# Performance work log

Measured on AMD Instinct MI355X. Metric: run time of the kernel, lower is better.

Reference implementation:

```python
import jax, jax.numpy as jnp
import numpy as np

N_NODES = 100000
N_EDGES = 3200000
H, D = 3, 12  # heads, per-head dim; H*D == node_hidden_dim == 36
NEG_SLOPE = 0.2


def setup_inputs() -> dict:
    key = jax.random.key(0)
    ks = jax.random.split(key, 11)
    s = 0.1
    return {
        "node_features": jax.random.normal(ks[0], (N_NODES, 36), jnp.float32),
        "src": jax.random.randint(ks[1], (N_EDGES,), 0, N_NODES),
        "dst": jax.random.randint(ks[2], (N_EDGES,), 0, N_NODES),
        "lin0_w": jax.random.normal(ks[3], (36, 36), jnp.float32) * s,
        "lin0_b": jax.random.normal(ks[4], (36,), jnp.float32) * s,
        "fc_w": jax.random.normal(ks[5], (3, 36, 36), jnp.float32) * s,
        "attn_l": jax.random.normal(ks[6], (3, H, D), jnp.float32) * s,
        "attn_r": jax.random.normal(ks[7], (3, H, D), jnp.float32) * s,
        "gat_bias": jax.random.normal(ks[8], (3, 36), jnp.float32) * s,
        "out_w": jax.random.normal(ks[9], (36, 36), jnp.float32) * s,
        "out_b": jax.random.normal(ks[10], (36,), jnp.float32) * s,
    }


def _gat_layer(h, src, dst, fc_w, a_l, a_r, bias):
    n = h.shape[0]
    feat = (h @ fc_w).reshape(n, H, D)                      # (N,H,D)
    el = jnp.sum(feat * a_l, axis=-1)                       # (N,H)
    er = jnp.sum(feat * a_r, axis=-1)                       # (N,H)
    e = el[src] + er[dst]                                   # (E,H)
    e = jnp.where(e >= 0, e, NEG_SLOPE * e)                 # leaky_relu(0.2)
    # edge softmax over incoming edges of each dst node (numerically stable)
    m = jax.ops.segment_max(e, dst, num_segments=n)         # (N,H)
    m = jnp.where(jnp.isfinite(m), m, 0.0)                  # zero-degree guard
    ee = jnp.exp(e - m[dst])                                # (E,H)
    denom = jax.ops.segment_sum(ee, dst, num_segments=n)    # (N,H)
    alpha = ee / jnp.maximum(denom[dst], 1e-9)              # (E,H)
    msg = feat[src] * alpha[:, :, None]                     # (E,H,D)
    rst = jax.ops.segment_sum(msg, dst, num_segments=n)     # (N,H,D)
    # residual (Identity since in_feats == H*D) + bias, then ELU
    rst = rst + h.reshape(n, H, D) + bias.reshape(1, H, D)
    return jax.nn.elu(rst).reshape(n, H * D)


def reference(node_features, src, dst, lin0_w, lin0_b, fc_w, attn_l, attn_r, gat_bias, out_w, out_b):
    h = node_features @ lin0_w + lin0_b
    for l in range(3):
        h = _gat_layer(h, src, dst, fc_w[l], attn_l[l], attn_r[l], gat_bias[l])
    return h @ out_w + out_b
```

## Files before the change

### kernel.cpp

```cpp
#include <hip/hip_runtime.h>
#include <math.h>

#define HID 36
#define NH 3
#define HD 12
#define BSHIFT 13
#define NBUCK 13
#define PSHIFT 8
#define PCHUNK 8192
#define CSRCAP 4096

typedef _Float16 f16;


__global__ void hist2_kernel(const int* __restrict__ dst, int* __restrict__ M,
                             int E, int C, int np) {
    __shared__ int h[512];
    int t = threadIdx.x;
    int c = blockIdx.x;
    for (int i = t; i < 512; i += blockDim.x) h[i] = 0;
    __syncthreads();
    int i0 = c * PCHUNK;
    int i1 = min(i0 + PCHUNK, E);
    for (int i = i0 + t; i < i1; i += blockDim.x)
        atomicAdd(&h[dst[i] >> PSHIFT], 1);
    __syncthreads();
    for (int b = t; b < np; b += blockDim.x)
        M[(size_t)b * C + c] = h[b];
}

__global__ void base_scan_kernel(const int* __restrict__ M, int* __restrict__ BaseT,
                                 int* __restrict__ T, int C, int np) {
    __shared__ int tmp[512];
    int b = blockIdx.x;
    int t = threadIdx.x;
    int v = (t < C) ? M[(size_t)b * C + t] : 0;
    tmp[t] = v;
    __syncthreads();
    for (int ofs = 1; ofs < 512; ofs <<= 1) {
        int x = 0;
        if (t >= ofs) x = tmp[t - ofs];
        __syncthreads();
        tmp[t] += x;
        __syncthreads();
    }
    if (t < C) BaseT[(size_t)t * 512 + b] = tmp[t] - v;
    if (t == 511) T[b] = tmp[511];
}

__global__ void scan_small_kernel(const int* __restrict__ T, int* __restrict__ poff, int np) {
    __shared__ int tmp[512];
    int t = threadIdx.x;
    int v = (t < np) ? T[t] : 0;
    tmp[t] = v;
    __syncthreads();
    for (int ofs = 1; ofs < 512; ofs <<= 1) {
        int x = 0;
        if (t >= ofs) x = tmp[t - ofs];
        __syncthreads();
        tmp[t] += x;
        __syncthreads();
    }
    int excl = tmp[t] - v;
    if (t < np) poff[t] = excl;
    if (t == np - 1) poff[np] = excl + v;
}

__global__ void part_scatter_kernel(const int* __restrict__ src, const int* __restrict__ dst,
                                    const int* __restrict__ BaseT, const int* __restrict__ poff,
                                    int* __restrict__ part, int E, int np) {
    __shared__ int h[512];
    __shared__ int base[512];
    int t = threadIdx.x;
    int c = blockIdx.x;
    for (int i = t; i < 512; i += blockDim.x) h[i] = 0;
    for (int b = t; b < np; b += blockDim.x)
        base[b] = poff[b] + BaseT[(size_t)c * 512 + b];
    __syncthreads();
    int i0 = c * PCHUNK;
    int i1 = min(i0 + PCHUNK, E);
    for (int i = i0 + t; i < i1; i += blockDim.x) {
        int d = dst[i];
        int bin = d >> PSHIFT;
        int r = atomicAdd(&h[bin], 1);
        part[base[bin] + r] = (src[i] << PSHIFT) | (d & ((1 << PSHIFT) - 1));
    }
}

__global__ void bucket_csr_kernel(const int* __restrict__ part, const int* __restrict__ T,
                                  const int* __restrict__ poff,
                                  int* __restrict__ csr, int* __restrict__ off,
                                  int n, int E) {
    __shared__ int cnt[256 * NBUCK];
    __shared__ int psum[256];
    int p = blockIdx.x;
    int t = threadIdx.x;
    int dbase = p << PSHIFT;
    int nd = min(256, n - dbase);
    int nc = nd * NBUCK;
    for (int i = t; i < nc; i += blockDim.x) cnt[i] = 0;
    __syncthreads();
    int cnt_p = T[p];
    int e0 = poff[p];
    const int* pp = part + e0;
    for (int i = t; i < cnt_p; i += blockDim.x) {
        int e = pp[i];
        atomicAdd(&cnt[(e & 255) * NBUCK + ((e >> PSHIFT) >> BSHIFT)], 1);
    }
    __syncthreads();
    int sum = 0;
    if (t < nd) {
        for (int k = 0; k < NBUCK; ++k) {
            int c = cnt[t * NBUCK + k];
            cnt[t * NBUCK + k] = sum;
            sum += c;
        }
    }
    psum[t] = (t < nd) ? sum : 0;
    __syncthreads();
    for (int ofs = 1; ofs < 256; ofs <<= 1) {
        int x = 0;
        if (t >= ofs) x = psum[t - ofs];
        __syncthreads();
        psum[t] += x;
        __syncthreads();
    }
    int dexcl = (t > 0) ? psum[t - 1] : 0;
    int start = e0 + dexcl;
    if (t < nd) {
        for (int k = 0; k < NBUCK; ++k) cnt[t * NBUCK + k] += start;
        off[dbase + t] = start;
    }
    __syncthreads();
    for (int i = t; i < cnt_p; i += blockDim.x) {
        int e = pp[i];
        int s = e >> PSHIFT;
        int idx = (e & 255) * NBUCK + (s >> BSHIFT);
        int pos = atomicAdd(&cnt[idx], 1);
        csr[pos] = s * 48;
    }
    if (p == 0 && t == 0) off[n] = E;
}


__device__ __forceinline__ void edge_accum(uint4 qa, uint4 qb, float ern,
                                           float& denom, float* acc) {
    union { uint4 q[2]; f16 hx[16]; } v;
    v.q[0] = qa;
    v.q[1] = qb;
    float e = (float)v.hx[12] + ern;
    e = (e >= 0.f) ? e : 0.2f * e;
    float w = __expf(e);
    denom += w;
#pragma unroll
    for (int k = 0; k < HD; ++k) acc[k] += w * (float)v.hx[k];
}

template <bool FITS>
__device__ __forceinline__ void sweep_edges(const int* __restrict__ smbuf,
                                            const int* __restrict__ csre,
                                            int j, int jend, const f16* __restrict__ pb,
                                            float ern, float& denom, float* acc) {
    int m = jend - j;
    for (; m >= 4; m -= 4, j += 4) {
        int o0 = FITS ? smbuf[j]     : csre[j];
        int o1 = FITS ? smbuf[j + 1] : csre[j + 1];
        int o2 = FITS ? smbuf[j + 2] : csre[j + 2];
        int o3 = FITS ? smbuf[j + 3] : csre[j + 3];
        const uint4* r0 = (const uint4*)(pb + o0);
        const uint4* r1 = (const uint4*)(pb + o1);
        const uint4* r2 = (const uint4*)(pb + o2);
        const uint4* r3 = (const uint4*)(pb + o3);
        uint4 a0 = r0[0], b0 = r0[1];
        uint4 a1 = r1[0], b1 = r1[1];
        uint4 a2 = r2[0], b2 = r2[1];
        uint4 a3 = r3[0], b3 = r3[1];
        edge_accum(a0, b0, ern, denom, acc);
        edge_accum(a1, b1, ern, denom, acc);
        edge_accum(a2, b2, ern, denom, acc);
        edge_accum(a3, b3, ern, denom, acc);
    }
    for (; m > 0; --m, ++j) {
        int o = FITS ? smbuf[j] : csre[j];
        const uint4* r = (const uint4*)(pb + o);
        edge_accum(r[0], r[1], ern, denom, acc);
    }
}

__global__ void lin0tr_kernel(const float* __restrict__ x, const float* __restrict__ w0,
                              const float* __restrict__ b0, const float* __restrict__ fcw,
                              const float* __restrict__ al, const float* __restrict__ ar,
                              float* __restrict__ h, f16* __restrict__ packed,
                              float* __restrict__ er, int n) {
    __shared__ float W0[HID * HID];
    __shared__ float W1[HID * HID];
    __shared__ float Bs[HID], ALs[HID], ARs[HID];
    int t = threadIdx.x;
    for (int i = t; i < HID * HID; i += 256) { W0[i] = w0[i]; W1[i] = fcw[i]; }
    if (t < HID) { Bs[t] = b0[t]; ALs[t] = al[t]; ARs[t] = ar[t]; }
    __syncthreads();
    int node = blockIdx.x * 256 + t;
    if (node >= n) return;
    const float4* xp = (const float4*)(x + (size_t)node * HID);
    float h0[HID];
#pragma unroll
    for (int j = 0; j < HID; ++j) h0[j] = Bs[j];
#pragma unroll
    for (int kk = 0; kk < HID / 4; ++kk) {
        float4 xv = xp[kk];
        const float* w = &W0[(4 * kk) * HID];
#pragma unroll
        for (int j = 0; j < HID; ++j)
            h0[j] += xv.x * w[j] + xv.y * w[HID + j] + xv.z * w[2 * HID + j] + xv.w * w[3 * HID + j];
    }
    float* hp = h + (size_t)node * HID;
#pragma unroll
    for (int j = 0; j < HID; ++j) hp[j] = h0[j];
    float feat[HID];
#pragma unroll
    for (int j = 0; j < HID; ++j) feat[j] = 0.f;
#pragma unroll
    for (int k = 0; k < HID; ++k) {
        float hv = h0[k];
        const float* w = &W1[k * HID];
#pragma unroll
        for (int j = 0; j < HID; ++j) feat[j] += hv * w[j];
    }
    union { f16 hx[48]; uint4 q[6]; } u;
#pragma unroll
    for (int hh = 0; hh < NH; ++hh) {
        float sl = 0.f, sr = 0.f;
#pragma unroll
        for (int d = 0; d < HD; ++d) {
            sl += feat[hh * HD + d] * ALs[hh * HD + d];
            sr += feat[hh * HD + d] * ARs[hh * HD + d];
        }
#pragma unroll
        for (int d = 0; d < HD; ++d) u.hx[hh * 16 + d] = (f16)feat[hh * HD + d];
        u.hx[hh * 16 + 12] = (f16)sl;
        u.hx[hh * 16 + 13] = (f16)0.f;
        u.hx[hh * 16 + 14] = (f16)0.f;
        u.hx[hh * 16 + 15] = (f16)0.f;
        er[node * NH + hh] = sr;
    }
    uint4* prow = (uint4*)(packed + (size_t)node * 48);
#pragma unroll
    for (int q = 0; q < 6; ++q) prow[q] = u.q[q];
}

__global__ void __launch_bounds__(192)
aggtr_kernel(const f16* __restrict__ packed_in, const float* __restrict__ er_in,
             const float* __restrict__ hcur,
             const int* __restrict__ off, const int* __restrict__ csr,
             const float* __restrict__ bias, const float* __restrict__ wnext,
             const float* __restrict__ aln, const float* __restrict__ arn,
             float* __restrict__ hnext, f16* __restrict__ packed_out,
             float* __restrict__ er_out, int n) {
    __shared__ float Wsh[HID * HID];
    __shared__ float ALs[HID], ARs[HID];
    __shared__ int smbuf[CSRCAP];
    int t = threadIdx.x;
    for (int i = t; i < HID * HID; i += 192) Wsh[i] = wnext[i];
    if (t < HID) { ALs[t] = aln[t]; ARs[t] = arn[t]; }
    int ln = t / 3, hh = t - ln * 3;
    int nb0 = blockIdx.x * 64;
    int node = nb0 + ln;
    bool active = (node < n);

    int e0 = off[nb0];
    int e1 = off[min(nb0 + 64, n)];
    int span = e1 - e0;
    bool fits = (span <= CSRCAP);
    if (fits)
        for (int i = t; i < span; i += 192) smbuf[i] = csr[e0 + i];

    int j0 = 0, j1 = 0;
    float ern = 0.f;
    if (active) {
        j0 = off[node] - e0;
        j1 = off[node + 1] - e0;
        ern = er_in[node * NH + hh];
    }
    const f16* pb = packed_in + hh * 16;
    __syncthreads();

    float denom = 0.f;
    float acc[HD];
#pragma unroll
    for (int k = 0; k < HD; ++k) acc[k] = 0.f;

    if (fits) sweep_edges<true>(smbuf, csr + e0, j0, j1, pb, ern, denom, acc);
    else      sweep_edges<false>(smbuf, csr + e0, j0, j1, pb, ern, denom, acc);
    __syncthreads();

    float* hsh = (float*)smbuf;
    float v[HD];
#pragma unroll
    for (int k = 0; k < HD; ++k) v[k] = 0.f;
    if (active) {
        float inv = 1.f / fmaxf(denom, 1e-9f);
        int base = node * HID + hh * HD;
        const float4* hc = (const float4*)(hcur + base);
        float4 h0 = hc[0], h1 = hc[1], h2 = hc[2];
        float hres[HD] = {h0.x, h0.y, h0.z, h0.w, h1.x, h1.y, h1.z, h1.w, h2.x, h2.y, h2.z, h2.w};
#pragma unroll
        for (int k = 0; k < HD; ++k) {
            float x = acc[k] * inv + hres[k] + bias[hh * HD + k];
            v[k] = (x > 0.f) ? x : expm1f(x);
        }
        float4* hp = (float4*)(hnext + base);
        hp[0] = make_float4(v[0], v[1], v[2], v[3]);
        hp[1] = make_float4(v[4], v[5], v[6], v[7]);
        hp[2] = make_float4(v[8], v[9], v[10], v[11]);
    }
#pragma unroll
    for (int k = 0; k < HD; ++k) hsh[ln * 37 + hh * HD + k] = v[k];
    __syncthreads();

    float feat[HD];
#pragma unroll
    for (int d = 0; d < HD; ++d) feat[d] = 0.f;
    const float* hrow = &hsh[ln * 37];
#pragma unroll 4
    for (int k = 0; k < HID; ++k) {
        float hv = hrow[k];
        const float* w = &Wsh[k * HID + hh * HD];
#pragma unroll
        for (int d = 0; d < HD; ++d) feat[d] += hv * w[d];
    }
    if (!active) return;
    float sl = 0.f, sr = 0.f;
#pragma unroll
    for (int d = 0; d < HD; ++d) {
        sl += feat[d] * ALs[hh * HD + d];
        sr += feat[d] * ARs[hh * HD + d];
    }
    union { f16 hx[16]; uint4 q[2]; } o;
#pragma unroll
    for (int d = 0; d < HD; ++d) o.hx[d] = (f16)feat[d];
    o.hx[12] = (f16)sl;
    o.hx[13] = (f16)0.f; o.hx[14] = (f16)0.f; o.hx[15] = (f16)0.f;
    uint4* prow = (uint4*)(packed_out + (size_t)node * 48 + hh * 16);
    prow[0] = o.q[0];
    prow[1] = o.q[1];
    er_out[node * NH + hh] = sr;
}

__global__ void __launch_bounds__(192)
aggout_kernel(const f16* __restrict__ packed_in, const float* __restrict__ er_in,
              const float* __restrict__ hcur,
              const int* __restrict__ off, const int* __restrict__ csr,
              const float* __restrict__ bias, const float* __restrict__ ow,
              const float* __restrict__ ob, float* __restrict__ out, int n) {
    __shared__ float Wsh[HID * HID];
    __shared__ float OBs[HID];
    __shared__ int smbuf[CSRCAP];
    int t = threadIdx.x;
    for (int i = t; i < HID * HID; i += 192) Wsh[i] = ow[i];
    if (t < HID) OBs[t] = ob[t];
    int ln = t / 3, hh = t - ln * 3;
    int nb0 = blockIdx.x * 64;
    int node = nb0 + ln;
    bool active = (node < n);

    int e0 = off[nb0];
    int e1 = off[min(nb0 + 64, n)];
    int span = e1 - e0;
    bool fits = (span <= CSRCAP);
    if (fits)
        for (int i = t; i < span; i += 192) smbuf[i] = csr[e0 + i];

    int j0 = 0, j1 = 0;
    float ern = 0.f;
    if (active) {
        j0 = off[node] - e0;
        j1 = off[node + 1] - e0;
        ern = er_in[node * NH + hh];
    }
    const f16* pb = packed_in + hh * 16;
    __syncthreads();

    float denom = 0.f;
    float acc[HD];
#pragma unroll
    for (int k = 0; k < HD; ++k) acc[k] = 0.f;

    if (fits) sweep_edges<true>(smbuf, csr + e0, j0, j1, pb, ern, denom, acc);
    else      sweep_edges<false>(smbuf, csr + e0, j0, j1, pb, ern, denom, acc);
    __syncthreads();

    float* hsh = (float*)smbuf;
    float v[HD];
#pragma unroll
    for (int k = 0; k < HD; ++k) v[k] = 0.f;
    if (active) {
        float inv = 1.f / fmaxf(denom, 1e-9f);
        int base = node * HID + hh * HD;
        const float4* hc = (const float4*)(hcur + base);
        float4 h0 = hc[0], h1 = hc[1], h2 = hc[2];
        float hres[HD] = {h0.x, h0.y, h0.z, h0.w, h1.x, h1.y, h1.z, h1.w, h2.x, h2.y, h2.z, h2.w};
#pragma unroll
        for (int k = 0; k < HD; ++k) {
            float x = acc[k] * inv + hres[k] + bias[hh * HD + k];
            v[k] = (x > 0.f) ? x : expm1f(x);
        }
    }
#pragma unroll
    for (int k = 0; k < HD; ++k) hsh[ln * 37 + hh * HD + k] = v[k];
    __syncthreads();

    float feat[HD];
#pragma unroll
    for (int d = 0; d < HD; ++d) feat[d] = OBs[hh * HD + d];
    const float* hrow = &hsh[ln * 37];
#pragma unroll 4
    for (int k = 0; k < HID; ++k) {
        float hv = hrow[k];
        const float* w = &Wsh[k * HID + hh * HD];
#pragma unroll
        for (int d = 0; d < HD; ++d) feat[d] += hv * w[d];
    }
    if (!active) return;
    float4* op = (float4*)(out + (size_t)node * HID + hh * HD);
    op[0] = make_float4(feat[0], feat[1], feat[2], feat[3]);
    op[1] = make_float4(feat[4], feat[5], feat[6], feat[7]);
    op[2] = make_float4(feat[8], feat[9], feat[10], feat[11]);
}


extern "C" void kernel_launch(void* const* d_in, const int* in_sizes, int n_in,
                              void* d_out, int out_size, void* d_ws, size_t ws_size,
                              hipStream_t stream) {
    const float* xnf = (const float*)d_in[0];
    const int* src = (const int*)d_in[1];
    const int* dst = (const int*)d_in[2];
    const float* l0w = (const float*)d_in[3];
    const float* l0b = (const float*)d_in[4];
    const float* fcw = (const float*)d_in[5];
    const float* al  = (const float*)d_in[6];
    const float* ar  = (const float*)d_in[7];
    const float* gb  = (const float*)d_in[8];
    const float* ow  = (const float*)d_in[9];
    const float* ob  = (const float*)d_in[10];
    float* out = (float*)d_out;
    const int N = in_sizes[0] / HID;
    const int E = in_sizes[1];
    const int NP = (N + (1 << PSHIFT) - 1) >> PSHIFT;
    const int C = (E + PCHUNK - 1) / PCHUNK;

    char* p = (char*)d_ws;
    auto alloc = [&](size_t bytes) {
        char* r = p;
        p += (bytes + 255) & ~(size_t)255;
        return r;
    };
    int* part    = (int*)alloc((size_t)E * 4);
    int* M       = (int*)alloc((size_t)NP * C * 4);
    int* BaseT   = (int*)alloc((size_t)C * 512 * 4);
    int* T       = (int*)alloc((size_t)NP * 4);
    int* poff    = (int*)alloc((size_t)(NP + 1) * 4);
    int* off     = (int*)alloc((size_t)(N + 1) * 4);
    int* csr     = (int*)alloc((size_t)E * 4);
    float* ha    = (float*)alloc((size_t)N * HID * 4);
    float* hb    = (float*)alloc((size_t)N * HID * 4);
    f16* pkA     = (f16*)alloc((size_t)N * 48 * 2);
    f16* pkB     = (f16*)alloc((size_t)N * 48 * 2);
    float* erA   = (float*)alloc((size_t)N * NH * 4);
    float* erB   = (float*)alloc((size_t)N * NH * 4);

    hist2_kernel<<<C, 256, 0, stream>>>(dst, M, E, C, NP);
    base_scan_kernel<<<NP, 512, 0, stream>>>(M, BaseT, T, C, NP);
    scan_small_kernel<<<1, 512, 0, stream>>>(T, poff, NP);
    part_scatter_kernel<<<C, 256, 0, stream>>>(src, dst, BaseT, poff, part, E, NP);
    bucket_csr_kernel<<<NP, 256, 0, stream>>>(part, T, poff, csr, off, N, E);

    int nblk = (N + 255) / 256;
    int fblk = (N + 63) / 64;

    lin0tr_kernel<<<nblk, 256, 0, stream>>>(xnf, l0w, l0b, fcw, al, ar, ha, pkA, erA, N);

    aggtr_kernel<<<fblk, 192, 0, stream>>>(pkA, erA, ha, off, csr, gb,
                                           fcw + (size_t)1 * HID * HID, al + HID, ar + HID,
                                           hb, pkB, erB, N);
    aggtr_kernel<<<fblk, 192, 0, stream>>>(pkB, erB, hb, off, csr, gb + HID,
                                           fcw + (size_t)2 * HID * HID, al + 2 * HID, ar + 2 * HID,
                                           ha, pkA, erA, N);
    aggout_kernel<<<fblk, 192, 0, stream>>>(pkA, erA, ha, off, csr, gb + 2 * HID,
                                            ow, ob, out, N);
}
```

Baseline: 388.8 us.

## Split each node-head edge sweep across two threads with shuffle reduction

The aggregation kernels now give each (node, head) pair two threads instead of one. The threads take alternating edges, and their partial softmax denominators and accumulators are combined with an xor shuffle. Blocks grow from 192 to 384 threads, and only the even lane runs the epilogue and the next-layer transform. The aim is more memory-level parallelism on the gather-heavy edge sweep, since degree averages about 32. The cost is extra shuffle work and half-idle threads in the epilogue.

```diff
diff --git a/kernel.cpp b/kernel.cpp
--- a/kernel.cpp
+++ b/kernel.cpp
@@ -157,16 +157,15 @@
 }
 
 template <bool FITS>
-__device__ __forceinline__ void sweep_edges(const int* __restrict__ smbuf,
-                                            const int* __restrict__ csre,
-                                            int j, int jend, const f16* __restrict__ pb,
-                                            float ern, float& denom, float* acc) {
-    int m = jend - j;
-    for (; m >= 4; m -= 4, j += 4) {
+__device__ __forceinline__ void sweep2(const int* __restrict__ smbuf,
+                                       const int* __restrict__ csre,
+                                       int j, int j1, const f16* __restrict__ pb,
+                                       float ern, float& denom, float* acc) {
+    for (; j + 6 < j1; j += 8) {
         int o0 = FITS ? smbuf[j]     : csre[j];
-        int o1 = FITS ? smbuf[j + 1] : csre[j + 1];
-        int o2 = FITS ? smbuf[j + 2] : csre[j + 2];
-        int o3 = FITS ? smbuf[j + 3] : csre[j + 3];
+        int o1 = FITS ? smbuf[j + 2] : csre[j + 2];
+        int o2 = FITS ? smbuf[j + 4] : csre[j + 4];
+        int o3 = FITS ? smbuf[j + 6] : csre[j + 6];
         const uint4* r0 = (const uint4*)(pb + o0);
         const uint4* r1 = (const uint4*)(pb + o1);
         const uint4* r2 = (const uint4*)(pb + o2);
@@ -180,7 +179,7 @@
         edge_accum(a2, b2, ern, denom, acc);
         edge_accum(a3, b3, ern, denom, acc);
     }
-    for (; m > 0; --m, ++j) {
+    for (; j < j1; j += 2) {
         int o = FITS ? smbuf[j] : csre[j];
         const uint4* r = (const uint4*)(pb + o);
         edge_accum(r[0], r[1], ern, denom, acc);
@@ -248,7 +247,7 @@
     for (int q = 0; q < 6; ++q) prow[q] = u.q[q];
 }
 
-__global__ void __launch_bounds__(192)
+__global__ void __launch_bounds__(384)
 aggtr_kernel(const f16* __restrict__ packed_in, const float* __restrict__ er_in,
              const float* __restrict__ hcur,
              const int* __restrict__ off, const int* __restrict__ csr,
@@ -260,9 +259,11 @@
     __shared__ float ALs[HID], ARs[HID];
     __shared__ int smbuf[CSRCAP];
     int t = threadIdx.x;
-    for (int i = t; i < HID * HID; i += 192) Wsh[i] = wnext[i];
+    for (int i = t; i < HID * HID; i += 384) Wsh[i] = wnext[i];
     if (t < HID) { ALs[t] = aln[t]; ARs[t] = arn[t]; }
-    int ln = t / 3, hh = t - ln * 3;
+    int s = t & 1;
+    int r = t >> 1;
+    int ln = r / 3, hh = r - ln * 3;
     int nb0 = blockIdx.x * 64;
     int node = nb0 + ln;
     bool active = (node < n);
@@ -272,16 +273,17 @@
     int span = e1 - e0;
     bool fits = (span <= CSRCAP);
     if (fits)
-        for (int i = t; i < span; i += 192) smbuf[i] = csr[e0 + i];
-
-    int j0 = 0, j1 = 0;
+        for (int i = t; i < span; i += 384) smbuf[i] = csr[e0 + i];
+
+    int j = 0, j1 = 0;
     float ern = 0.f;
     if (active) {
-        j0 = off[node] - e0;
+        j = off[node] - e0 + s;
         j1 = off[node + 1] - e0;
         ern = er_in[node * NH + hh];
     }
     const f16* pb = packed_in + hh * 16;
+    const int* csre = csr + e0;
     __syncthreads();
 
     float denom = 0.f;
@@ -289,33 +291,42 @@
 #pragma unroll
     for (int k = 0; k < HD; ++k) acc[k] = 0.f;
 
-    if (fits) sweep_edges<true>(smbuf, csr + e0, j0, j1, pb, ern, denom, acc);
-    else      sweep_edges<false>(smbuf, csr + e0, j0, j1, pb, ern, denom, acc);
+    if (fits) sweep2<true>(smbuf, csre, j, j1, pb, ern, denom, acc);
+    else      sweep2<false>(smbuf, csre, j, j1, pb, ern, denom, acc);
+
+    denom += __shfl_xor(denom, 1);
+#pragma unroll
+    for (int k = 0; k < HD; ++k) acc[k] += __shfl_xor(acc[k], 1);
+
     __syncthreads();
 
     float* hsh = (float*)smbuf;
-    float v[HD];
-#pragma unroll
-    for (int k = 0; k < HD; ++k) v[k] = 0.f;
-    if (active) {
-        float inv = 1.f / fmaxf(denom, 1e-9f);
-        int base = node * HID + hh * HD;
-        const float4* hc = (const float4*)(hcur + base);
-        float4 h0 = hc[0], h1 = hc[1], h2 = hc[2];
-        float hres[HD] = {h0.x, h0.y, h0.z, h0.w, h1.x, h1.y, h1.z, h1.w, h2.x, h2.y, h2.z, h2.w};
-#pragma unroll
-        for (int k = 0; k < HD; ++k) {
-            float x = acc[k] * inv + hres[k] + bias[hh * HD + k];
-            v[k] = (x > 0.f) ? x : expm1f(x);
+    if (s == 0) {
+        float v[HD];
+#pragma unroll
+        for (int k = 0; k < HD; ++k) v[k] = 0.f;
+        if (active) {
+            float inv = 1.f / fmaxf(denom, 1e-9f);
+            int base = node * HID + hh * HD;
+            const float4* hc = (const float4*)(hcur + base);
+            float4 h0 = hc[0], h1 = hc[1], h2 = hc[2];
+            float hres[HD] = {h0.x, h0.y, h0.z, h0.w, h1.x, h1.y, h1.z, h1.w,
+                              h2.x, h2.y, h2.z, h2.w};
+#pragma unroll
+            for (int k = 0; k < HD; ++k) {
+                float x = acc[k] * inv + hres[k] + bias[hh * HD + k];
+                v[k] = (x > 0.f) ? x : expm1f(x);
+            }
+            float4* hp = (float4*)(hnext + base);
+            hp[0] = make_float4(v[0], v[1], v[2], v[3]);
+            hp[1] = make_float4(v[4], v[5], v[6], v[7]);
+            hp[2] = make_float4(v[8], v[9], v[10], v[11]);
         }
-        float4* hp = (float4*)(hnext + base);
-        hp[0] = make_float4(v[0], v[1], v[2], v[3]);
-        hp[1] = make_float4(v[4], v[5], v[6], v[7]);
-        hp[2] = make_float4(v[8], v[9], v[10], v[11]);
-    }
-#pragma unroll
-    for (int k = 0; k < HD; ++k) hsh[ln * 37 + hh * HD + k] = v[k];
-    __syncthreads();
+#pragma unroll
+        for (int k = 0; k < HD; ++k) hsh[ln * 37 + hh * HD + k] = v[k];
+    }
+    __syncthreads();
+    if (s) return;
 
     float feat[HD];
 #pragma unroll
@@ -346,7 +357,7 @@
     er_out[node * NH + hh] = sr;
 }
 
-__global__ void __launch_bounds__(192)
+__global__ void __launch_bounds__(384)
 aggout_kernel(const f16* __restrict__ packed_in, const float* __restrict__ er_in,
               const float* __restrict__ hcur,
               const int* __restrict__ off, const int* __restrict__ csr,
@@ -356,9 +367,11 @@
     __shared__ float OBs[HID];
     __shared__ int smbuf[CSRCAP];
     int t = threadIdx.x;
-    for (int i = t; i < HID * HID; i += 192) Wsh[i] = ow[i];
+    for (int i = t; i < HID * HID; i += 384) Wsh[i] = ow[i];
     if (t < HID) OBs[t] = ob[t];
-    int ln = t / 3, hh = t - ln * 3;
+    int s = t & 1;
+    int r = t >> 1;
+    int ln = r / 3, hh = r - ln * 3;
     int nb0 = blockIdx.x * 64;
     int node = nb0 + ln;
     bool active = (node < n);
@@ -368,16 +381,17 @@
     int span = e1 - e0;
     bool fits = (span <= CSRCAP);
     if (fits)
-        for (int i = t; i < span; i += 192) smbuf[i] = csr[e0 + i];
-
-    int j0 = 0, j1 = 0;
+        for (int i = t; i < span; i += 384) smbuf[i] = csr[e0 + i];
+
+    int j = 0, j1 = 0;
     float ern = 0.f;
     if (active) {
-        j0 = off[node] - e0;
+        j = off[node] - e0 + s;
         j1 = off[node + 1] - e0;
         ern = er_in[node * NH + hh];
     }
     const f16* pb = packed_in + hh * 16;
+    const int* csre = csr + e0;
     __syncthreads();
 
     float denom = 0.f;
@@ -385,29 +399,38 @@
 #pragma unroll
     for (int k = 0; k < HD; ++k) acc[k] = 0.f;
 
-    if (fits) sweep_edges<true>(smbuf, csr + e0, j0, j1, pb, ern, denom, acc);
-    else      sweep_edges<false>(smbuf, csr + e0, j0, j1, pb, ern, denom, acc);
+    if (fits) sweep2<true>(smbuf, csre, j, j1, pb, ern, denom, acc);
+    else      sweep2<false>(smbuf, csre, j, j1, pb, ern, denom, acc);
+
+    denom += __shfl_xor(denom, 1);
+#pragma unroll
+    for (int k = 0; k < HD; ++k) acc[k] += __shfl_xor(acc[k], 1);
+
     __syncthreads();
 
     float* hsh = (float*)smbuf;
-    float v[HD];
-#pragma unroll
-    for (int k = 0; k < HD; ++k) v[k] = 0.f;
-    if (active) {
-        float inv = 1.f / fmaxf(denom, 1e-9f);
-        int base = node * HID + hh * HD;
-        const float4* hc = (const float4*)(hcur + base);
-        float4 h0 = hc[0], h1 = hc[1], h2 = hc[2];
-        float hres[HD] = {h0.x, h0.y, h0.z, h0.w, h1.x, h1.y, h1.z, h1.w, h2.x, h2.y, h2.z, h2.w};
-#pragma unroll
-        for (int k = 0; k < HD; ++k) {
-            float x = acc[k] * inv + hres[k] + bias[hh * HD + k];
-            v[k] = (x > 0.f) ? x : expm1f(x);
+    if (s == 0) {
+        float v[HD];
+#pragma unroll
+        for (int k = 0; k < HD; ++k) v[k] = 0.f;
+        if (active) {
+            float inv = 1.f / fmaxf(denom, 1e-9f);
+            int base = node * HID + hh * HD;
+            const float4* hc = (const float4*)(hcur + base);
+            float4 h0 = hc[0], h1 = hc[1], h2 = hc[2];
+            float hres[HD] = {h0.x, h0.y, h0.z, h0.w, h1.x, h1.y, h1.z, h1.w,
+                              h2.x, h2.y, h2.z, h2.w};
+#pragma unroll
+            for (int k = 0; k < HD; ++k) {
+                float x = acc[k] * inv + hres[k] + bias[hh * HD + k];
+                v[k] = (x > 0.f) ? x : expm1f(x);
+            }
         }
-    }
-#pragma unroll
-    for (int k = 0; k < HD; ++k) hsh[ln * 37 + hh * HD + k] = v[k];
-    __syncthreads();
+#pragma unroll
+        for (int k = 0; k < HD; ++k) hsh[ln * 37 + hh * HD + k] = v[k];
+    }
+    __syncthreads();
+    if (s) return;
 
     float feat[HD];
 #pragma unroll
@@ -479,12 +502,12 @@
 
     lin0tr_kernel<<<nblk, 256, 0, stream>>>(xnf, l0w, l0b, fcw, al, ar, ha, pkA, erA, N);
 
-    aggtr_kernel<<<fblk, 192, 0, stream>>>(pkA, erA, ha, off, csr, gb,
+    aggtr_kernel<<<fblk, 384, 0, stream>>>(pkA, erA, ha, off, csr, gb,
                                            fcw + (size_t)1 * HID * HID, al + HID, ar + HID,
                                            hb, pkB, erB, N);
-    aggtr_kernel<<<fblk, 192, 0, stream>>>(pkB, erB, hb, off, csr, gb + HID,
+    aggtr_kernel<<<fblk, 384, 0, stream>>>(pkB, erB, hb, off, csr, gb + HID,
                                            fcw + (size_t)2 * HID * HID, al + 2 * HID, ar + 2 * HID,
                                            ha, pkA, erA, N);
-    aggout_kernel<<<fblk, 192, 0, stream>>>(pkA, erA, ha, off, csr, gb + 2 * HID,
+    aggout_kernel<<<fblk, 384, 0, stream>>>(pkA, erA, ha, off, csr, gb + 2 * HID,
                                             ow, ob, out, N);
 }
```

New measurement: 454.5 us. 16.9% more time.
